# Optimization experiments

Measured on AMD Instinct MI355X. Metric: run time of the kernel, lower is better.

## Reference

```python
import jax, jax.numpy as jnp
import numpy as np
import math

B, S, HID = 2, 2048, 1024
NH, HD = 16, 64  # num_heads, head_dim = HID // NH


def setup_inputs() -> dict:
    key = jax.random.key(0)
    ks = jax.random.split(key, 12)
    sc = 1.0 / math.sqrt(HID)
    inp = {
        "x": jax.random.normal(ks[0], (B, S, HID), dtype=jnp.float32),
        "time_deltas": jax.random.uniform(ks[1], (B, S), dtype=jnp.float32),
        # torch.nn.Linear weights are [out, in]; y = x @ W.T + b
        "Wq": jax.random.normal(ks[2], (HID, HID), dtype=jnp.float32) * sc,
        "bq": jnp.zeros((HID,), dtype=jnp.float32),
        "Wk": jax.random.normal(ks[3], (HID, HID), dtype=jnp.float32) * sc,
        "bk": jnp.zeros((HID,), dtype=jnp.float32),
        "Wv": jax.random.normal(ks[4], (HID, HID), dtype=jnp.float32) * sc,
        "bv": jnp.zeros((HID,), dtype=jnp.float32),
        "Wo": jax.random.normal(ks[5], (HID, HID), dtype=jnp.float32) * sc,
        "bo": jnp.zeros((HID,), dtype=jnp.float32),
        "time_decay": jnp.ones((NH,), dtype=jnp.float32),
    }
    return inp


def reference(x, time_deltas, Wq, bq, Wk, bk, Wv, bv, Wo, bo, time_decay):
    b, s, _ = x.shape

    def heads(W, bias):
        # [b, s, hid] -> [b, nh, s, hd]
        return (x @ W.T + bias).reshape(b, s, NH, HD).transpose(0, 2, 1, 3)

    q = heads(Wq, bq)
    k = heads(Wk, bk)
    v = heads(Wv, bv)

    scores = jnp.einsum("bhqd,bhkd->bhqk", q, k) / math.sqrt(HD)

    # pairwise |t_i - t_j| decay bias, per-head learned rate
    tm = jnp.abs(time_deltas[:, :, None] - time_deltas[:, None, :])  # [b, s, s]
    decay = jnp.exp(-time_decay[None, :, None, None] * tm[:, None, :, :])
    scores = scores * decay

    causal = jnp.triu(jnp.ones((s, s), dtype=bool), k=1)  # True above diagonal
    scores = jnp.where(causal[None, None], -jnp.inf, scores)

    attn = jax.nn.softmax(scores, axis=-1)  # dropout is identity at inference
    out = jnp.einsum("bhqk,bhkd->bhqd", attn, v)
    out = out.transpose(0, 2, 1, 3).reshape(b, s, HID)
    return out @ Wo.T + bo
```

## Files before the change

kernel.cpp:

```cpp
#include <hip/hip_runtime.h>
#include <hip/hip_bf16.h>

typedef __attribute__((ext_vector_type(4))) float f32x4;
typedef __attribute__((ext_vector_type(8))) __bf16 bf16x8;
typedef __attribute__((ext_vector_type(4))) unsigned short us4;

static constexpr int BB = 2, SS = 2048, HID = 1024, NH = 16, HD = 64;
static constexpr int M_TOT = BB * SS;

static __device__ __forceinline__ f32x4 mfma16(bf16x8 a, bf16x8 b, f32x4 c) {
  return __builtin_amdgcn_mfma_f32_16x16x32_bf16(a, b, c, 0, 0, 0);
}

static __device__ __forceinline__ unsigned short f2b(float x) {
  __hip_bfloat16 h = __float2bfloat16(x);
  unsigned short u;
  __builtin_memcpy(&u, &h, 2);
  return u;
}

static __device__ __forceinline__ float ex2(float x) {
  return __builtin_amdgcn_exp2f(x);
}

__global__ void cvt_all(const float* __restrict__ x,  const float* __restrict__ wq,
                        const float* __restrict__ wk, const float* __restrict__ wv,
                        const float* __restrict__ wo,
                        unsigned short* __restrict__ xb,  unsigned short* __restrict__ wqb,
                        unsigned short* __restrict__ wkb, unsigned short* __restrict__ wvb,
                        unsigned short* __restrict__ wob) {
  int y = blockIdx.y;
  const float* s; unsigned short* d; int n4;
  if (y == 0)      { s = x;  d = xb;  n4 = M_TOT * HID / 4; }
  else if (y == 1) { s = wq; d = wqb; n4 = HID * HID / 4; }
  else if (y == 2) { s = wk; d = wkb; n4 = HID * HID / 4; }
  else if (y == 3) { s = wv; d = wvb; n4 = HID * HID / 4; }
  else             { s = wo; d = wob; n4 = HID * HID / 4; }
  int idx = blockIdx.x * blockDim.x + threadIdx.x;
  int stride = gridDim.x * blockDim.x;
  const f32x4* sv = (const f32x4*)s;
  us4* dv = (us4*)d;
  for (int i = idx; i < n4; i += stride) {
    f32x4 v = sv[i];
    us4 o;
    o.x = f2b(v.x); o.y = f2b(v.y); o.z = f2b(v.z); o.w = f2b(v.w);
    dv[i] = o;
  }
}

static __device__ __forceinline__ void stage_ab(
    const unsigned short* __restrict__ gA, const unsigned short* __restrict__ gB,
    int k0, unsigned short* As, unsigned short* Bs, int t) {
#pragma unroll
  for (int i_ = 0; i_ < 4; ++i_) {
    int chunk = i_ * 256 + t;
    int row = chunk >> 3;
    int col = (chunk & 7) << 3;
    __builtin_amdgcn_global_load_lds(
        (const __attribute__((address_space(1))) unsigned int*)(gA + (size_t)row * HID + k0 + col),
        (__attribute__((address_space(3))) unsigned int*)(As + chunk * 8), 16, 0, 0);
    __builtin_amdgcn_global_load_lds(
        (const __attribute__((address_space(1))) unsigned int*)(gB + (size_t)row * HID + k0 + col),
        (__attribute__((address_space(3))) unsigned int*)(Bs + chunk * 8), 16, 0, 0);
  }
}

static __device__ __forceinline__ void gemm_mainloop(
    const unsigned short* __restrict__ gA,
    const unsigned short* __restrict__ gB,
    unsigned short* As, unsigned short* Bs,
    int t, f32x4 acc[4][4]) {
  const int l = t & 63;
  const int lr = l & 15, lg = (l >> 4) & 3;
  const int w = t >> 6;
  const int wr = w >> 1, wc = w & 1;
  stage_ab(gA, gB, 0, As, Bs, t);
  int cur = 0;
  for (int k0 = 0; k0 < HID; k0 += 64) {
    if (k0 + 64 < HID) {
      stage_ab(gA, gB, k0 + 64, As + (cur ^ 1) * 8192, Bs + (cur ^ 1) * 8192, t);
      asm volatile("s_waitcnt vmcnt(8)" ::: "memory");
    } else {
      asm volatile("s_waitcnt vmcnt(0)" ::: "memory");
    }
    __builtin_amdgcn_s_barrier();
    asm volatile("" ::: "memory");
    const unsigned short* Ac = As + cur * 8192;
    const unsigned short* Bc = Bs + cur * 8192;
#pragma unroll
    for (int kk = 0; kk < 2; ++kk) {
      bf16x8 a[4], bb[4];
#pragma unroll
      for (int mf = 0; mf < 4; ++mf)
        a[mf] = *(const bf16x8*)&Ac[(wr * 64 + mf * 16 + lr) * 64 + kk * 32 + lg * 8];
#pragma unroll
      for (int nf = 0; nf < 4; ++nf)
        bb[nf] = *(const bf16x8*)&Bc[(wc * 64 + nf * 16 + lr) * 64 + kk * 32 + lg * 8];
#pragma unroll
      for (int mf = 0; mf < 4; ++mf)
#pragma unroll
        for (int nf = 0; nf < 4; ++nf)
          acc[mf][nf] = mfma16(a[mf], bb[nf], acc[mf][nf]);
    }
    asm volatile("" ::: "memory");
    __builtin_amdgcn_s_barrier();
    cur ^= 1;
  }
}

__global__ __launch_bounds__(256, 2) void qkv_gemm(
    const unsigned short* __restrict__ xb,
    const unsigned short* __restrict__ wqb, const unsigned short* __restrict__ wkb,
    const unsigned short* __restrict__ wvb,
    const float* __restrict__ bq, const float* __restrict__ bk, const float* __restrict__ bv,
    unsigned short* __restrict__ qo, unsigned short* __restrict__ ko,
    unsigned short* __restrict__ vto) {
  __shared__ unsigned short As[2 * 128 * 64];
  __shared__ unsigned short Bs[2 * 128 * 64];
  int t = threadIdx.x;
  int z = blockIdx.z;
  const unsigned short* Bmat = (z == 0) ? wqb : (z == 1) ? wkb : wvb;
  const float* bias = (z == 0) ? bq : (z == 1) ? bk : bv;
  int m0 = blockIdx.y * 128, n0 = blockIdx.x * 128;
  f32x4 acc[4][4] = {};
  gemm_mainloop(xb + (size_t)m0 * HID, Bmat + (size_t)n0 * HID, As, Bs, t, acc);

  int l = t & 63, lr = l & 15, lg = (l >> 4) & 3;
  int w = t >> 6, wr = w >> 1, wc = w & 1;
  float scale = (z == 0) ? 0.125f : 1.0f;
#pragma unroll
  for (int nf = 0; nf < 4; ++nf) {
    int n = n0 + wc * 64 + nf * 16 + lr;
    float bs = bias[n];
    int h = n >> 6, d = n & 63;
#pragma unroll
    for (int mf = 0; mf < 4; ++mf) {
#pragma unroll
      for (int j = 0; j < 4; ++j) {
        int m = m0 + wr * 64 + mf * 16 + lg * 4 + j;
        int b = m >> 11, sidx = m & (SS - 1);
        float val = (acc[mf][nf][j] + bs) * scale;
        unsigned short ob = f2b(val);
        if (z == 2)
          vto[((size_t)(b * NH + h) * HD + d) * SS + sidx] = ob;
        else {
          unsigned short* dst = (z == 0) ? qo : ko;
          dst[((size_t)(b * NH + h) * SS + sidx) * HD + d] = ob;
        }
      }
    }
  }
}

__global__ __launch_bounds__(256, 2) void out_gemm(
    const unsigned short* __restrict__ Ab,
    const unsigned short* __restrict__ Wb,
    const float* __restrict__ bias,
    float* __restrict__ C) {
  __shared__ unsigned short As[2 * 128 * 64];
  __shared__ unsigned short Bs[2 * 128 * 64];
  int t = threadIdx.x;
  int m0 = blockIdx.y * 128, n0 = blockIdx.x * 128;
  f32x4 acc[4][4] = {};
  gemm_mainloop(Ab + (size_t)m0 * HID, Wb + (size_t)n0 * HID, As, Bs, t, acc);

  int l = t & 63, lr = l & 15, lg = (l >> 4) & 3;
  int w = t >> 6, wr = w >> 1, wc = w & 1;
#pragma unroll
  for (int nf = 0; nf < 4; ++nf) {
    int n = n0 + wc * 64 + nf * 16 + lr;
    float bs = bias[n];
#pragma unroll
    for (int mf = 0; mf < 4; ++mf) {
#pragma unroll
      for (int j = 0; j < 4; ++j) {
        int m = m0 + wr * 64 + mf * 16 + lg * 4 + j;
        C[(size_t)m * HID + n] = acc[mf][nf][j] + bs;
      }
    }
  }
}

static __device__ __forceinline__ void stage_kv(
    const unsigned short* __restrict__ kp, const unsigned short* __restrict__ vp,
    int kv0, unsigned short* Kd, unsigned short* Vd, int t) {
#pragma unroll
  for (int i_ = 0; i_ < 2; ++i_) {
    int chunk = i_ * 256 + t;
    int row = chunk >> 3;
    int srcc = ((chunk & 7) ^ (row & 7)) << 3;
    __builtin_amdgcn_global_load_lds(
        (const __attribute__((address_space(1))) unsigned int*)(kp + (size_t)(kv0 + row) * HD + srcc),
        (__attribute__((address_space(3))) unsigned int*)(Kd + chunk * 8), 16, 0, 0);
    __builtin_amdgcn_global_load_lds(
        (const __attribute__((address_space(1))) unsigned int*)(vp + (size_t)row * SS + kv0 + srcc),
        (__attribute__((address_space(3))) unsigned int*)(Vd + chunk * 8), 16, 0, 0);
  }
}

__global__ __launch_bounds__(256, 2) void attn_kernel(
    const unsigned short* __restrict__ qg,
    const unsigned short* __restrict__ kg,
    const unsigned short* __restrict__ vtg,
    const float* __restrict__ td,
    const float* __restrict__ decay,
    unsigned short* __restrict__ outb) {
  __shared__ unsigned short Ks[2][64 * 64];
  __shared__ unsigned short Vs[2][64 * 64];
  __shared__ unsigned short Pl[4][16][64];
  const int t = threadIdx.x;
  const int l = t & 63;
  const int w = t >> 6;
  const int lr = l & 15, lg = (l >> 4) & 3;
  const int L = blockIdx.x;
  const int W = (L & 7) * 64 + (L >> 3);
  const int xp = W & 15;
  const int h = (W >> 4) & 15;
  const int b = W >> 8;
  const unsigned short* qp = qg + ((size_t)(b * NH + h) * SS) * HD;
  const unsigned short* kp = kg + ((size_t)(b * NH + h) * SS) * HD;
  const unsigned short* vp = vtg + ((size_t)(b * NH + h) * HD) * SS;
  const float* tdb = td + (size_t)b * SS;
  const float dec = decay[h];
  const float L2E = 1.44269504f;
  const float dl = dec * L2E;
  const float SHIFT = 16.0f;

  for (int seg = 0; seg < 2; ++seg) {
    const int qb = seg ? 31 - xp : xp;
    const int q0 = qb * 64;
    const int qw = q0 + w * 16;

    bf16x8 qf0 = *(const bf16x8*)&qp[(size_t)(qw + lr) * HD + lg * 8];
    bf16x8 qf1 = *(const bf16x8*)&qp[(size_t)(qw + lr) * HD + 32 + lg * 8];
    float eqL[4], fqL[4];
#pragma unroll
    for (int j = 0; j < 4; ++j) {
      float tq = tdb[qw + lg * 4 + j];
      eqL[j] = ex2(dl * tq) * L2E;
      fqL[j] = ex2(-dl * tq) * L2E;
    }
    float lsum[4] = {0.f, 0.f, 0.f, 0.f};
    f32x4 o[4] = {};

    stage_kv(kp, vp, 0, Ks[0], Vs[0], t);
    int cur = 0;
    for (int tkv = 0; tkv <= qb; ++tkv) {
      const int kv0 = tkv * 64;
      if (tkv < qb) {
        stage_kv(kp, vp, kv0 + 64, Ks[cur ^ 1], Vs[cur ^ 1], t);
        asm volatile("s_waitcnt vmcnt(4)" ::: "memory");
      } else {
        asm volatile("s_waitcnt vmcnt(0)" ::: "memory");
      }
      __builtin_amdgcn_s_barrier();
      asm volatile("" ::: "memory");
      const unsigned short* Kc = Ks[cur];
      const unsigned short* Vc = Vs[cur];

      f32x4 s[4];
#pragma unroll
      for (int nf = 0; nf < 4; ++nf) {
        int r = nf * 16 + lr;
        bf16x8 kf0 = *(const bf16x8*)&Kc[r * 64 + ((lg ^ (r & 7)) << 3)];
        bf16x8 kf1 = *(const bf16x8*)&Kc[r * 64 + (((4 + lg) ^ (r & 7)) << 3)];
        f32x4 zz = {};
        zz = mfma16(qf0, kf0, zz);
        s[nf] = mfma16(qf1, kf1, zz);
      }
      const bool diag = (tkv == qb);
#pragma unroll
      for (int nf = 0; nf < 4; ++nf) {
        int col = kv0 + nf * 16 + lr;
        float tk = tdb[col];
        float ek = ex2(dl * tk);
        float fk = ex2(-dl * tk);
#pragma unroll
        for (int j = 0; j < 4; ++j) {
          int row = lg * 4 + j;
          float wL = fminf(eqL[j] * fk, fqL[j] * ek);
          float pv = ex2(s[nf][j] * wL - SHIFT);
          if (diag && col > qw + row) pv = 0.f;
          lsum[j] += pv;
          Pl[w][row][(nf * 16 + lr) ^ ((row & 7) << 3)] = f2b(pv);
        }
      }
#pragma unroll
      for (int kk = 0; kk < 2; ++kk) {
        bf16x8 pa = *(const bf16x8*)&Pl[w][lr][(kk * 32 + lg * 8) ^ ((lr & 7) << 3)];
        int g = kk * 4 + lg;
#pragma unroll
        for (int df = 0; df < 4; ++df) {
          int r = df * 16 + lr;
          bf16x8 vf = *(const bf16x8*)&Vc[r * 64 + ((g ^ (r & 7)) << 3)];
          o[df] = mfma16(pa, vf, o[df]);
        }
      }
      __syncthreads();
      cur ^= 1;
    }
#pragma unroll
    for (int j = 0; j < 4; ++j) {
      float rs = lsum[j];
      rs += __shfl_xor(rs, 1, 16);
      rs += __shfl_xor(rs, 2, 16);
      rs += __shfl_xor(rs, 4, 16);
      rs += __shfl_xor(rs, 8, 16);
      float inv = 1.0f / rs;
      int srow = qw + lg * 4 + j;
#pragma unroll
      for (int df = 0; df < 4; ++df)
        outb[((size_t)b * SS + srow) * HID + h * HD + df * 16 + lr] = f2b(o[df][j] * inv);
    }
  }
}

extern "C" void kernel_launch(void* const* d_in, const int* in_sizes, int n_in,
                              void* d_out, int out_size, void* d_ws, size_t ws_size,
                              hipStream_t stream) {
  const float* x    = (const float*)d_in[0];
  const float* td   = (const float*)d_in[1];
  const float* Wq   = (const float*)d_in[2];
  const float* bq   = (const float*)d_in[3];
  const float* Wk   = (const float*)d_in[4];
  const float* bk   = (const float*)d_in[5];
  const float* Wv   = (const float*)d_in[6];
  const float* bv   = (const float*)d_in[7];
  const float* Wo   = (const float*)d_in[8];
  const float* bo   = (const float*)d_in[9];
  const float* tdec = (const float*)d_in[10];
  float* out = (float*)d_out;

  char* ws = (char*)d_ws;
  unsigned short* xb  = (unsigned short*)ws; ws += (size_t)M_TOT * HID * 2;
  unsigned short* wqb = (unsigned short*)ws; ws += (size_t)HID * HID * 2;
  unsigned short* wkb = (unsigned short*)ws; ws += (size_t)HID * HID * 2;
  unsigned short* wvb = (unsigned short*)ws; ws += (size_t)HID * HID * 2;
  unsigned short* wob = (unsigned short*)ws; ws += (size_t)HID * HID * 2;
  unsigned short* qb  = (unsigned short*)ws; ws += (size_t)M_TOT * HID * 2;
  unsigned short* kb  = (unsigned short*)ws; ws += (size_t)M_TOT * HID * 2;
  unsigned short* vtb = (unsigned short*)ws; ws += (size_t)M_TOT * HID * 2;
  unsigned short* ob  = (unsigned short*)ws; ws += (size_t)M_TOT * HID * 2;

  cvt_all<<<dim3(512, 5), 256, 0, stream>>>(x, Wq, Wk, Wv, Wo, xb, wqb, wkb, wvb, wob);
  qkv_gemm<<<dim3(HID / 128, M_TOT / 128, 3), 256, 0, stream>>>(
      xb, wqb, wkb, wvb, bq, bk, bv, qb, kb, vtb);
  attn_kernel<<<512, 256, 0, stream>>>(qb, kb, vtb, td, tdec, ob);
  out_gemm<<<dim3(HID / 128, M_TOT / 128), 256, 0, stream>>>(ob, wob, bo, out);
}
```

Before: 227.6 us.

## XOR-swizzle GEMM LDS tiles and drop double buffering to single-stage loads

The GEMM staging now writes each 16-byte chunk of a row into LDS with an XOR swizzle on the column index, and the fragment reads apply the same swizzle. This is meant to remove LDS bank conflicts on the MFMA operand loads. At the same time the double-buffered prefetch pipeline is removed: each k-step loads its tile, synchronises, computes and synchronises again, with half the shared memory. That may allow more resident blocks, but global-load latency is no longer overlapped with compute.

```diff
diff --git a/kernel.cpp b/kernel.cpp
--- a/kernel.cpp
+++ b/kernel.cpp
@@ -55,12 +55,12 @@
   for (int i_ = 0; i_ < 4; ++i_) {
     int chunk = i_ * 256 + t;
     int row = chunk >> 3;
-    int col = (chunk & 7) << 3;
+    int srcc = ((chunk & 7) ^ (row & 7)) << 3;
     __builtin_amdgcn_global_load_lds(
-        (const __attribute__((address_space(1))) unsigned int*)(gA + (size_t)row * HID + k0 + col),
+        (const __attribute__((address_space(1))) unsigned int*)(gA + (size_t)row * HID + k0 + srcc),
         (__attribute__((address_space(3))) unsigned int*)(As + chunk * 8), 16, 0, 0);
     __builtin_amdgcn_global_load_lds(
-        (const __attribute__((address_space(1))) unsigned int*)(gB + (size_t)row * HID + k0 + col),
+        (const __attribute__((address_space(1))) unsigned int*)(gB + (size_t)row * HID + k0 + srcc),
         (__attribute__((address_space(3))) unsigned int*)(Bs + chunk * 8), 16, 0, 0);
   }
 }
@@ -68,43 +68,34 @@
 static __device__ __forceinline__ void gemm_mainloop(
     const unsigned short* __restrict__ gA,
     const unsigned short* __restrict__ gB,
-    unsigned short* As, unsigned short* Bs,
-    int t, f32x4 acc[4][4]) {
+    unsigned short* As, unsigned short* Bs, int t, f32x4 acc[4][4]) {
   const int l = t & 63;
   const int lr = l & 15, lg = (l >> 4) & 3;
   const int w = t >> 6;
   const int wr = w >> 1, wc = w & 1;
-  stage_ab(gA, gB, 0, As, Bs, t);
-  int cur = 0;
   for (int k0 = 0; k0 < HID; k0 += 64) {
-    if (k0 + 64 < HID) {
-      stage_ab(gA, gB, k0 + 64, As + (cur ^ 1) * 8192, Bs + (cur ^ 1) * 8192, t);
-      asm volatile("s_waitcnt vmcnt(8)" ::: "memory");
-    } else {
-      asm volatile("s_waitcnt vmcnt(0)" ::: "memory");
-    }
-    __builtin_amdgcn_s_barrier();
-    asm volatile("" ::: "memory");
-    const unsigned short* Ac = As + cur * 8192;
-    const unsigned short* Bc = Bs + cur * 8192;
+    stage_ab(gA, gB, k0, As, Bs, t);
+    __syncthreads();
 #pragma unroll
     for (int kk = 0; kk < 2; ++kk) {
       bf16x8 a[4], bb[4];
 #pragma unroll
-      for (int mf = 0; mf < 4; ++mf)
-        a[mf] = *(const bf16x8*)&Ac[(wr * 64 + mf * 16 + lr) * 64 + kk * 32 + lg * 8];
-#pragma unroll
-      for (int nf = 0; nf < 4; ++nf)
-        bb[nf] = *(const bf16x8*)&Bc[(wc * 64 + nf * 16 + lr) * 64 + kk * 32 + lg * 8];
+      for (int mf = 0; mf < 4; ++mf) {
+        int r = wr * 64 + mf * 16 + lr;
+        a[mf] = *(const bf16x8*)&As[r * 64 + (((kk * 4 + lg) ^ (lr & 7)) << 3)];
+      }
+#pragma unroll
+      for (int nf = 0; nf < 4; ++nf) {
+        int r = wc * 64 + nf * 16 + lr;
+        bb[nf] = *(const bf16x8*)&Bs[r * 64 + (((kk * 4 + lg) ^ (lr & 7)) << 3)];
+      }
 #pragma unroll
       for (int mf = 0; mf < 4; ++mf)
 #pragma unroll
         for (int nf = 0; nf < 4; ++nf)
           acc[mf][nf] = mfma16(a[mf], bb[nf], acc[mf][nf]);
     }
-    asm volatile("" ::: "memory");
-    __builtin_amdgcn_s_barrier();
-    cur ^= 1;
+    __syncthreads();
   }
 }
 
@@ -115,8 +106,8 @@
     const float* __restrict__ bq, const float* __restrict__ bk, const float* __restrict__ bv,
     unsigned short* __restrict__ qo, unsigned short* __restrict__ ko,
     unsigned short* __restrict__ vto) {
-  __shared__ unsigned short As[2 * 128 * 64];
-  __shared__ unsigned short Bs[2 * 128 * 64];
+  __shared__ unsigned short As[128 * 64];
+  __shared__ unsigned short Bs[128 * 64];
   int t = threadIdx.x;
   int z = blockIdx.z;
   const unsigned short* Bmat = (z == 0) ? wqb : (z == 1) ? wkb : wvb;
@@ -157,8 +148,8 @@
     const unsigned short* __restrict__ Wb,
     const float* __restrict__ bias,
     float* __restrict__ C) {
-  __shared__ unsigned short As[2 * 128 * 64];
-  __shared__ unsigned short Bs[2 * 128 * 64];
+  __shared__ unsigned short As[128 * 64];
+  __shared__ unsigned short Bs[128 * 64];
   int t = threadIdx.x;
   int m0 = blockIdx.y * 128, n0 = blockIdx.x * 128;
   f32x4 acc[4][4] = {};
```

New measurement: 197.0 us. 13.5% less time.
